# Performance work log

Measured on AMD Instinct MI355X. Metric: run time of the kernel, lower is better.

Reference implementation:

```python
import jax, jax.numpy as jnp
import numpy as np

N_NODES = 50000
N_EDGES = 800000
N_GRAPHS = 64
EPS = 1e-5


def glorot(key, shape):
    fan_in, fan_out = shape[0], shape[1]
    lim = np.sqrt(6.0 / (fan_in + fan_out))
    return jax.random.uniform(key, shape, jnp.float32, -lim, lim)


def setup_inputs() -> dict:
    key = jax.random.key(0)
    ks = jax.random.split(key, 12)
    x = jax.random.normal(ks[0], (N_NODES, 1), jnp.float32)
    edge_index = jax.random.randint(ks[1], (2, N_EDGES), 0, N_NODES, jnp.int64)
    batch = jnp.sort(jax.random.randint(ks[2], (N_NODES,), 0, N_GRAPHS, jnp.int64))
    dims = [(1, 256), (256, 256), (256, 128)]
    params = {}
    for i, (di, do) in enumerate(dims):
        params[f"Wl{i}"] = glorot(ks[3 + 3 * i], (di, do))          # neighbor (lin_l) weight
        params[f"b{i}"] = jnp.zeros((do,), jnp.float32)              # lin_l bias
        params[f"Wr{i}"] = glorot(ks[4 + 3 * i], (di, do))           # root (lin_r) weight
    params["gamma"] = jnp.ones((128,), jnp.float32)
    params["beta"] = jnp.zeros((128,), jnp.float32)
    return {"x": x, "edge_index": edge_index, "batch": batch, **params}


def _sage_conv(x, src, dst, deg_inv, Wl, b, Wr):
    # mean-aggregate messages x[src] at dst, then lin_l(agg) + lin_r(x)
    agg = jax.ops.segment_sum(x[src], dst, num_segments=N_NODES) * deg_inv
    return agg @ Wl + b + x @ Wr


def reference(x, edge_index, batch, Wl0, b0, Wr0, Wl1, b1, Wr1, Wl2, b2, Wr2, gamma, beta):
    src, dst = edge_index[0], edge_index[1]
    deg = jax.ops.segment_sum(jnp.ones((N_EDGES,), x.dtype), dst, num_segments=N_NODES)
    deg_inv = (1.0 / jnp.maximum(deg, 1.0))[:, None]

    h = _sage_conv(x, src, dst, deg_inv, Wl0, b0, Wr0)
    h = jax.nn.relu(h)  # dropout is identity in eval mode
    h = _sage_conv(h, src, dst, deg_inv, Wl1, b1, Wr1)
    h = jax.nn.relu(h)
    h = _sage_conv(h, src, dst, deg_inv, Wl2, b2, Wr2)

    # global mean pool over graphs
    gsum = jax.ops.segment_sum(h, batch, num_segments=N_GRAPHS)
    gcnt = jax.ops.segment_sum(jnp.ones((N_NODES,), h.dtype), batch, num_segments=N_GRAPHS)
    g = gsum / jnp.maximum(gcnt, 1.0)[:, None]

    # LayerNorm over feature dim
    mu = jnp.mean(g, axis=-1, keepdims=True)
    var = jnp.var(g, axis=-1, keepdims=True)
    return (g - mu) * jax.lax.rsqrt(var + EPS) * gamma + beta
```

## Files before the change

kernel.cpp:

```cpp
#include <hip/hip_runtime.h>
#include <stdint.h>

#define NN 50000
#define NE 800000
#define NG 64
#define F1 256
#define NNP 50176
#define NBK 196
#define NBS 392
#define EPB 2048
#define SCB 391
#define PCHUNKS 112
#define PKC 448
#define PSTEPS 7
#define ZR2 128

typedef __bf16 bf16x8 __attribute__((ext_vector_type(8)));
typedef float f32x4 __attribute__((ext_vector_type(4)));

__device__ __forceinline__ float bf2f(unsigned int u) {
  union { float f; unsigned int i; } v; v.i = (u & 0xffffu) << 16; return v.f;
}
__device__ __forceinline__ unsigned short f2bf(float f) {
  union { float f; unsigned int i; } v; v.f = f;
  unsigned int r = v.i + 0x7fffu + ((v.i >> 16) & 1u);
  return (unsigned short)(r >> 16);
}
__device__ __forceinline__ float asf(unsigned int u) {
  union { unsigned int u; float f; } v; v.u = u; return v.f;
}
__device__ __forceinline__ unsigned int asu(float f) {
  union { float f; unsigned int u; } v; v.f = f; return v.u;
}
__device__ __forceinline__ void gload16(const void* g, void* l) {
  __builtin_amdgcn_global_load_lds(
      (const __attribute__((address_space(1))) unsigned int*)g,
      (__attribute__((address_space(3))) unsigned int*)l, 16, 0, 0);
}

__global__ void k_bhist(const int* __restrict__ ei, int* __restrict__ btot_d,
                        int* __restrict__ btot_s) {
  __shared__ int lhd[NBK];
  __shared__ int lhs[NBS];
  for (int i = threadIdx.x; i < NBK; i += 256) lhd[i] = 0;
  for (int i = threadIdx.x; i < NBS; i += 256) lhs[i] = 0;
  __syncthreads();
  for (int e = blockIdx.x * blockDim.x + threadIdx.x; e < NE; e += gridDim.x * blockDim.x) {
    atomicAdd(&lhs[ei[e] >> 7], 1);
    atomicAdd(&lhd[ei[NE + e] >> 8], 1);
  }
  __syncthreads();
  for (int i = threadIdx.x; i < NBK; i += 256) atomicAdd(&btot_d[i], lhd[i]);
  for (int i = threadIdx.x; i < NBS; i += 256) atomicAdd(&btot_s[i], lhs[i]);
}

__global__ void k_bscan(const int* __restrict__ btot_d, const int* __restrict__ btot_s,
                        int* __restrict__ bbase, int* __restrict__ bcur,
                        int* __restrict__ sbase, int* __restrict__ scur,
                        int* __restrict__ rowp) {
  __shared__ int buf[512];
  int t = threadIdx.x;
  int v = (t < NBK) ? btot_d[t] : 0;
  buf[t] = v;
  __syncthreads();
  for (int off = 1; off < 512; off <<= 1) {
    int o = (t >= off) ? buf[t - off] : 0;
    __syncthreads();
    buf[t] += o;
    __syncthreads();
  }
  if (t < NBK) { bbase[t] = buf[t] - v; bcur[t] = buf[t] - v; }
  if (t == NBK - 1) bbase[NBK] = buf[t];
  __syncthreads();
  int v2 = (t < NBS) ? btot_s[t] : 0;
  buf[t] = v2;
  __syncthreads();
  for (int off = 1; off < 512; off <<= 1) {
    int o = (t >= off) ? buf[t - off] : 0;
    __syncthreads();
    buf[t] += o;
    __syncthreads();
  }
  if (t < NBS) { sbase[t] = buf[t] - v2; scur[t] = buf[t] - v2; }
  if (t == NBS - 1) sbase[NBS] = buf[t];
  if (t == 0) rowp[NN] = NE;
}

__global__ __launch_bounds__(256) void k_bscatter(
    const int* __restrict__ ei, const float* __restrict__ x,
    int* __restrict__ bcur, int* __restrict__ scur,
    uint2* __restrict__ recs, unsigned int* __restrict__ srecs) {
  __shared__ int lhd[NBK]; __shared__ int gbd[NBK];
  __shared__ int lhs[NBS]; __shared__ int gbs[NBS];
  int b = blockIdx.x, tid = threadIdx.x;
  int e0 = b * EPB;
  for (int i = tid; i < NBK; i += 256) lhd[i] = 0;
  for (int i = tid; i < NBS; i += 256) lhs[i] = 0;
  __syncthreads();
  unsigned int meta[8]; float xv[8]; int lofd[8]; int bkd[8]; int lofs[8]; int bks[8];
#pragma unroll
  for (int i = 0; i < 8; ++i) {
    int e = e0 + i * 256 + tid;
    bkd[i] = -1;
    if (e < NE) {
      int s = ei[e], d = ei[NE + e];
      bkd[i] = d >> 8; bks[i] = s >> 7;
      meta[i] = (unsigned int)s | ((unsigned int)d << 16);
      xv[i] = x[s];
      lofd[i] = atomicAdd(&lhd[bkd[i]], 1);
      lofs[i] = atomicAdd(&lhs[bks[i]], 1);
    }
  }
  __syncthreads();
  for (int i = tid; i < NBK; i += 256) gbd[i] = atomicAdd(&bcur[i], lhd[i]);
  for (int i = tid; i < NBS; i += 256) gbs[i] = atomicAdd(&scur[i], lhs[i]);
  __syncthreads();
#pragma unroll
  for (int i = 0; i < 8; ++i) {
    if (bkd[i] >= 0) {
      recs[gbd[bkd[i]] + lofd[i]] = make_uint2(meta[i], asu(xv[i]));
      unsigned int s = meta[i] & 0xFFFFu, d = meta[i] >> 16;
      srecs[gbs[bks[i]] + lofs[i]] = d | ((s & 127u) << 16);
    }
  }
}

__global__ __launch_bounds__(256) void k_csr(
    const uint2* __restrict__ recs, const int* __restrict__ bbase,
    const float* __restrict__ x, const int* __restrict__ batch,
    int* __restrict__ rowp, float2* __restrict__ ax,
    int* __restrict__ colx, uint2* __restrict__ dg) {
  __shared__ int cnt[256];
  __shared__ int sc[256];
  __shared__ float xs[256];
  int b = blockIdx.x, tid = threadIdx.x;
  int eb = bbase[b], ee = bbase[b + 1];
  cnt[tid] = 0;
  xs[tid] = 0.0f;
  __syncthreads();
  for (int e = eb + tid; e < ee; e += 256) {
    uint2 r = recs[e];
    int dl = (r.x >> 16) & 255;
    atomicAdd(&cnt[dl], 1);
    atomicAdd(&xs[dl], asf(r.y));
  }
  __syncthreads();
  sc[tid] = cnt[tid];
  __syncthreads();
  for (int off = 1; off < 256; off <<= 1) {
    int o = (tid >= off) ? sc[tid - off] : 0;
    __syncthreads();
    sc[tid] += o;
    __syncthreads();
  }
  int excl = sc[tid] - cnt[tid];
  int i = b * 256 + tid;
  float dinv = 1.0f / fmaxf((float)cnt[tid], 1.0f);
  if (i < NN) {
    rowp[i] = eb + excl;
    ax[i] = make_float2(xs[tid] * dinv, x[i]);
    dg[i] = make_uint2(asu(dinv), (unsigned int)batch[i]);
  }
  __syncthreads();
  sc[tid] = excl;
  __syncthreads();
  for (int e = eb + tid; e < ee; e += 256) {
    uint2 r = recs[e];
    int dl = (r.x >> 16) & 255;
    int s = r.x & 0xFFFF;
    int slot = atomicAdd(&sc[dl], 1);
    colx[eb + slot] = s;
  }
}

__global__ __launch_bounds__(256) void k_csc(
    const unsigned int* __restrict__ srecs, const int* __restrict__ sbase,
    const uint2* __restrict__ dg, const int* __restrict__ batch,
    unsigned int* __restrict__ wgT3u) {
  __shared__ float wgrow[128 * 65];
  __shared__ int sbt[128];
  int b = blockIdx.x, tid = threadIdx.x;
  for (int i = tid; i < 128 * 65; i += 256) wgrow[i] = 0.0f;
  if (tid < 128) {
    int s = b * 128 + tid;
    sbt[tid] = (s < NN) ? batch[s] : -1;
  }
  __syncthreads();
  int eb = sbase[b], ee = sbase[b + 1];
  for (int e = eb + tid; e < ee; e += 256) {
    unsigned int r = srecs[e];
    int d = r & 0xFFFF;
    int sl = (r >> 16) & 127;
    uint2 t = dg[d];
    atomicAdd(&wgrow[sl * 65 + t.y], asf(t.x));
  }
  __syncthreads();
  int s0u = b * 64;
  int k = tid & 63;
  for (int rr = 0; rr < 16; ++rr) {
    int g = rr * 4 + (tid >> 6);
    float w0 = wgrow[(2 * k) * 65 + g];
    float w1 = wgrow[(2 * k + 1) * 65 + g];
    unsigned short h0 = f2bf(w0), h1v = f2bf(w1);
    unsigned short l0 = f2bf(w0 - bf2f(h0)), l1 = f2bf(w1 - bf2f(h1v));
    wgT3u[(size_t)g * (NNP / 2) + s0u + k] = (unsigned int)h0 | ((unsigned int)h1v << 16);
    wgT3u[(size_t)(64 + g) * (NNP / 2) + s0u + k] = (unsigned int)l0 | ((unsigned int)l1 << 16);
  }
  int bv0 = sbt[2 * k], bv1 = sbt[2 * k + 1];
  for (int rr = 0; rr < 16; ++rr) {
    int g = rr * 4 + (tid >> 6);
    unsigned int u = ((bv0 == g) ? 0x3F80u : 0u) | ((bv1 == g) ? 0x3F800000u : 0u);
    wgT3u[(size_t)(128 + g) * (NNP / 2) + s0u + k] = u;
  }
}

__global__ void k_cnt(const int* __restrict__ batch, int* __restrict__ cnt) {
  int g = threadIdx.x;
  if (g >= NG) return;
  int lo = 0, hi = NN;
  while (lo < hi) { int m = (lo + hi) >> 1; if (batch[m] < g) lo = m + 1; else hi = m; }
  int a = lo;
  lo = 0; hi = NN;
  while (lo < hi) { int m = (lo + hi) >> 1; if (batch[m] < g + 1) lo = m + 1; else hi = m; }
  cnt[g] = lo - a;
}

__global__ void k_axe(const int* __restrict__ colx, const float2* __restrict__ ax,
                      float2* __restrict__ axe) {
  int e = blockIdx.x * blockDim.x + threadIdx.x;
  if (e >= NE) return;
  axe[e] = ax[colx[e]];
}

__global__ void k_wprep(const float* __restrict__ Wl1, const float* __restrict__ Wr1,
                        unsigned short* __restrict__ wcat) {
  int t = blockIdx.x * blockDim.x + threadIdx.x;
  if (t >= 256 * 512) return;
  int n = t >> 9, k = t & 511;
  float v = (k < 256) ? Wl1[k * 256 + n] : Wr1[(k - 256) * 256 + n];
  wcat[t] = f2bf(v);
}

__global__ __launch_bounds__(256) void k_agg2(
    const float2* __restrict__ axe, const int* __restrict__ rowp,
    const float* __restrict__ Wl0, const float* __restrict__ b0,
    const float* __restrict__ Wr0, unsigned short* __restrict__ aggb) {
  int wid = threadIdx.x >> 6, lane = threadIdx.x & 63;
  int gw = blockIdx.x * 4 + wid;
  int tw = gridDim.x * 4;
  float wl[4], wr[4], bb[4];
#pragma unroll
  for (int k = 0; k < 4; ++k) {
    wl[k] = Wl0[lane * 4 + k];
    wr[k] = Wr0[lane * 4 + k];
    bb[k] = b0[lane * 4 + k];
  }
  for (int d = gw; d < NN; d += tw) {
    int beg = rowp[d], end = rowp[d + 1];
    float a[4] = {0.f, 0.f, 0.f, 0.f};
    float c[4] = {0.f, 0.f, 0.f, 0.f};
    int e = beg;
    for (; e + 3 < end; e += 4) {
      float2 v0 = axe[e], v1 = axe[e + 1], v2 = axe[e + 2], v3 = axe[e + 3];
#pragma unroll
      for (int k = 0; k < 4; ++k) {
        a[k] += fmaxf(fmaf(v0.x, wl[k], fmaf(v0.y, wr[k], bb[k])), 0.0f);
        c[k] += fmaxf(fmaf(v1.x, wl[k], fmaf(v1.y, wr[k], bb[k])), 0.0f);
        a[k] += fmaxf(fmaf(v2.x, wl[k], fmaf(v2.y, wr[k], bb[k])), 0.0f);
        c[k] += fmaxf(fmaf(v3.x, wl[k], fmaf(v3.y, wr[k], bb[k])), 0.0f);
      }
    }
    for (; e < end; ++e) {
      float2 v0 = axe[e];
#pragma unroll
      for (int k = 0; k < 4; ++k)
        a[k] += fmaxf(fmaf(v0.x, wl[k], fmaf(v0.y, wr[k], bb[k])), 0.0f);
    }
    float dinv = 1.0f / fmaxf((float)(end - beg), 1.0f);
    uint2 o;
    o.x = (unsigned int)f2bf((a[0] + c[0]) * dinv) | ((unsigned int)f2bf((a[1] + c[1]) * dinv) << 16);
    o.y = (unsigned int)f2bf((a[2] + c[2]) * dinv) | ((unsigned int)f2bf((a[3] + c[3]) * dinv) << 16);
    *(uint2*)(aggb + (size_t)d * F1 + lane * 4) = o;
  }
}

#define BM 128
#define BN 128
#define BK 32

__global__ __launch_bounds__(256) void k_gemm1(
    const unsigned short* __restrict__ aggb, const float2* __restrict__ ax,
    const unsigned short* __restrict__ wcat,
    const float* __restrict__ Wl0, const float* __restrict__ b0,
    const float* __restrict__ Wr0, const float* __restrict__ b1,
    unsigned short* __restrict__ h1T) {
  __shared__ unsigned short As[2][BM][BK];
  __shared__ unsigned short Bs[2][BN][BK];
  __shared__ float wl0s[256], wr0s[256], b0s[256];
  int bm = blockIdx.x, ct = blockIdx.y;
  int tid = threadIdx.x;
  int wid = tid >> 6, lane = tid & 63;
  int wr = wid >> 1, wc = wid & 1;
  int rc = lane & 15, kh = lane >> 4;
  int r0 = bm * BM;
  int srow = tid >> 1;
  int sslot = tid & 1;

  wl0s[tid] = Wl0[tid];
  wr0s[tid] = Wr0[tid];
  b0s[tid] = b0[tid];

  int rA = r0 + srow;
  bool rAok = rA < NN;
  float2 axv = rAok ? ax[rA] : make_float2(0.f, 0.f);

  f32x4 acc[4][4] = {};
  int4 ra0, ra1, rb0, rb1;

#define LOAD_A(kt)                                                             \
  do {                                                                         \
    ra0 = make_int4(0, 0, 0, 0); ra1 = make_int4(0, 0, 0, 0);                  \
    if (rAok) {                                                                \
      const int4* s_ = (const int4*)(aggb + (size_t)rA * F1 + (kt) * BK + sslot * 16); \
      ra0 = s_[0]; ra1 = s_[1];                                                \
    }                                                                          \
  } while (0)

#define LOAD_B(kt)                                                             \
  do {                                                                         \
    const int4* t_ = (const int4*)(wcat + (size_t)(ct * BN + srow) * 512 + (kt) * BK + sslot * 16); \
    rb0 = t_[0]; rb1 = t_[1];                                                  \
  } while (0)

#define COMP_A(kt)                                                             \
  do {                                                                         \
    int j0_ = ((kt) - 8) * BK + sslot * 16;                                    \
    unsigned int w_[8];                                                        \
    _Pragma("unroll") for (int q = 0; q < 8; ++q) {                            \
      int j_ = j0_ + 2 * q;                                                    \
      float f0_ = fmaxf(fmaf(axv.x, wl0s[j_], fmaf(axv.y, wr0s[j_], b0s[j_])), 0.0f); \
      float f1_ = fmaxf(fmaf(axv.x, wl0s[j_ + 1], fmaf(axv.y, wr0s[j_ + 1], b0s[j_ + 1])), 0.0f); \
      w_[q] = (unsigned int)f2bf(f0_) | ((unsigned int)f2bf(f1_) << 16);       \
    }                                                                          \
    ra0 = make_int4(w_[0], w_[1], w_[2], w_[3]);                               \
    ra1 = make_int4(w_[4], w_[5], w_[6], w_[7]);                               \
  } while (0)

#define WRITE_AB(buf)                                                          \
  do {                                                                         \
    int sw_ = (srow >> 1) & 3;                                                 \
    int ws0_ = (2 * sslot) ^ sw_;                                              \
    int ws1_ = (2 * sslot + 1) ^ sw_;                                          \
    *(int4*)&As[buf][srow][ws0_ * 8] = ra0;                                    \
    *(int4*)&As[buf][srow][ws1_ * 8] = ra1;                                    \
    *(int4*)&Bs[buf][srow][ws0_ * 8] = rb0;                                    \
    *(int4*)&Bs[buf][srow][ws1_ * 8] = rb1;                                    \
  } while (0)

  LOAD_B(0);
  LOAD_A(0);
  WRITE_AB(0);
  __syncthreads();
  int cur = 0;
  for (int kt = 0; kt < 16; ++kt) {
    if (kt < 15) {
      LOAD_B(kt + 1);
      if (kt + 1 < 8) LOAD_A(kt + 1);
    }
    bf16x8 af[4], bfr[4];
#pragma unroll
    for (int mf = 0; mf < 4; ++mf) {
      int row = wr * 64 + mf * 16 + rc;
      int sl = kh ^ ((row >> 1) & 3);
      af[mf] = *(const bf16x8*)&As[cur][row][sl * 8];
    }
#pragma unroll
    for (int nf = 0; nf < 4; ++nf) {
      int row = wc * 64 + nf * 16 + rc;
      int sl = kh ^ ((row >> 1) & 3);
      bfr[nf] = *(const bf16x8*)&Bs[cur][row][sl * 8];
    }
#pragma unroll
    for (int mf = 0; mf < 4; ++mf)
#pragma unroll
      for (int nf = 0; nf < 4; ++nf)
        acc[mf][nf] = __builtin_amdgcn_mfma_f32_16x16x32_bf16(af[mf], bfr[nf], acc[mf][nf], 0, 0, 0);
    if (kt < 15) {
      if (kt + 1 >= 8) COMP_A(kt + 1);
      WRITE_AB(cur ^ 1);
    }
    __syncthreads();
    cur ^= 1;
  }
#undef LOAD_A
#undef LOAD_B
#undef COMP_A
#undef WRITE_AB

#pragma unroll
  for (int nf = 0; nf < 4; ++nf) {
    int f = ct * BN + wc * 64 + nf * 16 + rc;
    float bias = b1[f];
    size_t frow = (size_t)f * NNP;
#pragma unroll
    for (int mf = 0; mf < 4; ++mf) {
      int s0 = r0 + wr * 64 + mf * 16 + kh * 4;
      f32x4 a = acc[mf][nf];
      unsigned int lo = (unsigned int)f2bf(fmaxf(a[0] + bias, 0.0f)) |
                        ((unsigned int)f2bf(fmaxf(a[1] + bias, 0.0f)) << 16);
      unsigned int hi = (unsigned int)f2bf(fmaxf(a[2] + bias, 0.0f)) |
                        ((unsigned int)f2bf(fmaxf(a[3] + bias, 0.0f)) << 16);
      *(uint2*)(h1T + frow + s0) = make_uint2(lo, hi);
    }
  }
}

__global__ __launch_bounds__(256, 2) void k_poolmm(
    const unsigned short* __restrict__ h1T, const unsigned short* __restrict__ wgT3,
    float* __restrict__ zpart) {
  __shared__ unsigned short SM[2][2048 * 8];
  int bid = blockIdx.x;
  int lbid = (bid & 7) * 56 + (bid >> 3);
  int c = lbid >> 2, fs = lbid & 3;
  int tid = threadIdx.x;
  int w = tid >> 6, lane = tid & 63, rc = lane & 15, kh = lane >> 4;
  int kbase = c * PKC;
  int fbase = fs * 64;

  const unsigned short* gsrc[8];
#pragma unroll
  for (int r = 0; r < 8; ++r) {
    int sIdx = r * 256 + tid;
    if (sIdx < 1536) {
      int row = sIdx >> 3, sl = sIdx & 7;
      gsrc[r] = wgT3 + (size_t)row * NNP + kbase + (sl ^ (row & 7)) * 8;
    } else {
      int row = (sIdx - 1536) >> 3, sl = sIdx & 7;
      gsrc[r] = h1T + (size_t)(fbase + row) * NNP + kbase + (sl ^ (row & 7)) * 8;
    }
  }

  f32x4 acc[12] = {};

#define PSTAGE(buf, t)                                                         \
  do {                                                                         \
    _Pragma("unroll") for (int r = 0; r < 8; ++r)                              \
      gload16(gsrc[r] + (t) * 64, &SM[buf][(r * 256 + w * 64) * 8]);           \
  } while (0)

#define PCOMP(buf)                                                             \
  do {                                                                         \
    _Pragma("unroll") for (int ks = 0; ks < 2; ++ks) {                         \
      int brow = w * 16 + rc;                                                  \
      int bsl = (ks * 4 + kh) ^ (brow & 7);                                    \
      bf16x8 bf = *(const bf16x8*)&SM[buf][(1536 + brow * 8 + bsl) * 8];       \
      _Pragma("unroll") for (int mt = 0; mt < 12; ++mt) {                      \
        int arow = mt * 16 + rc;                                               \
        int asl = (ks * 4 + kh) ^ (arow & 7);                                  \
        bf16x8 af = *(const bf16x8*)&SM[buf][(arow * 8 + asl) * 8];            \
        acc[mt] = __builtin_amdgcn_mfma_f32_16x16x32_bf16(af, bf, acc[mt], 0, 0, 0); \
      }                                                                        \
    }                                                                          \
  } while (0)

  PSTAGE(0, 0);
  __syncthreads();
#pragma unroll
  for (int t = 0; t < PSTEPS; ++t) {
    int buf = t & 1;
    if (t + 1 < PSTEPS) PSTAGE(buf ^ 1, t + 1);
    PCOMP(buf);
    __syncthreads();
  }
#undef PSTAGE
#undef PCOMP

  float* zp = zpart + ((size_t)c * ZR2) * F1 + fbase + w * 16 + rc;
#pragma unroll
  for (int mt = 0; mt < 4; ++mt)
#pragma unroll
    for (int r = 0; r < 4; ++r)
      zp[(size_t)(mt * 16 + kh * 4 + r) * F1] = acc[mt][r] + acc[mt + 4][r];
#pragma unroll
  for (int mt = 8; mt < 12; ++mt)
#pragma unroll
    for (int r = 0; r < 4; ++r)
      zp[(size_t)((mt - 8) * 16 + 64 + kh * 4 + r) * F1] = acc[mt][r];
}

__global__ void k_zred(const float* __restrict__ zpart, float* __restrict__ z,
                       float* __restrict__ p1) {
  int g = blockIdx.x, q = blockIdx.y, t = threadIdx.x;
  float a = 0.0f, b = 0.0f;
  for (int c = q * 14; c < q * 14 + 14; ++c) {
    const float* base = zpart + (size_t)c * ZR2 * F1;
    a += base[(size_t)g * F1 + t];
    b += base[(size_t)(64 + g) * F1 + t];
  }
  atomicAdd(&z[g * F1 + t], a);
  atomicAdd(&p1[g * F1 + t], b);
}

__global__ void k_final(const float* __restrict__ z, const float* __restrict__ p1,
                        const int* __restrict__ cnt,
                        const float* __restrict__ Wl2, const float* __restrict__ b2,
                        const float* __restrict__ Wr2, const float* __restrict__ gamma,
                        const float* __restrict__ beta, float* __restrict__ out) {
  __shared__ float s1[128], s2[128];
  int g = blockIdx.x, j = threadIdx.x;
  float invc = 1.0f / fmaxf((float)cnt[g], 1.0f);
  float acc = 0.0f;
  for (int k = 0; k < 256; ++k) {
    acc += z[g * 256 + k] * Wl2[k * 128 + j] + p1[g * 256 + k] * Wr2[k * 128 + j];
  }
  acc = acc * invc + b2[j];
  s1[j] = acc; s2[j] = acc * acc;
  __syncthreads();
  for (int off = 64; off > 0; off >>= 1) {
    if (j < off) { s1[j] += s1[j + off]; s2[j] += s2[j + off]; }
    __syncthreads();
  }
  float mu = s1[0] / 128.0f;
  float var = s2[0] / 128.0f - mu * mu;
  out[g * 128 + j] = (acc - mu) * rsqrtf(var + 1e-5f) * gamma[j] + beta[j];
}

extern "C" void kernel_launch(void* const* d_in, const int* in_sizes, int n_in,
                              void* d_out, int out_size, void* d_ws, size_t ws_size,
                              hipStream_t stream) {
  const float* x = (const float*)d_in[0];
  const int* ei = (const int*)d_in[1];
  const int* batch = (const int*)d_in[2];
  const float* Wl0 = (const float*)d_in[3];
  const float* b0 = (const float*)d_in[4];
  const float* Wr0 = (const float*)d_in[5];
  const float* Wl1 = (const float*)d_in[6];
  const float* b1 = (const float*)d_in[7];
  const float* Wr1 = (const float*)d_in[8];
  const float* Wl2 = (const float*)d_in[9];
  const float* b2 = (const float*)d_in[10];
  const float* Wr2 = (const float*)d_in[11];
  const float* gamma = (const float*)d_in[12];
  const float* beta = (const float*)d_in[13];
  float* out = (float*)d_out;

  char* p = (char*)d_ws;
  auto alloc = [&](size_t bytes) {
    char* r = p;
    p += (bytes + 511) & ~(size_t)511;
    return r;
  };
  unsigned short* h1T = (unsigned short*)alloc((size_t)F1 * NNP * 2);
  unsigned short* aggb = (unsigned short*)alloc((size_t)NN * F1 * 2);
  float2* axe = (float2*)alloc((size_t)NE * 8);
  int* rowp = (int*)alloc((size_t)(NN + 1) * 4);
  float2* ax = (float2*)alloc((size_t)NN * 8);
  uint2* dg = (uint2*)alloc((size_t)NN * 8);
  int* cnt = (int*)alloc((size_t)NG * 4);
  float* z = (float*)alloc((size_t)NG * F1 * 4);
  float* p1 = (float*)alloc((size_t)NG * F1 * 4);
  unsigned short* wcat = (unsigned short*)alloc((size_t)256 * 512 * 2);
  int* btot_d = (int*)alloc((size_t)NBK * 4);
  int* btot_s = (int*)alloc((size_t)NBS * 4);
  int* bbase = (int*)alloc((size_t)(NBK + 1) * 4);
  int* bcur = (int*)alloc((size_t)NBK * 4);
  int* sbase = (int*)alloc((size_t)(NBS + 1) * 4);
  int* scur = (int*)alloc((size_t)NBS * 4);
  unsigned short* wgT3 = (unsigned short*)alloc((size_t)192 * NNP * 2);
  float* zpart = (float*)alloc((size_t)PCHUNKS * ZR2 * F1 * 4);
  uint2* recs = (uint2*)aggb;
  unsigned int* srecs = (unsigned int*)(aggb + (size_t)NE * 4);
  int* colx = (int*)(aggb + (size_t)NE * 6);

  hipMemsetAsync(btot_d, 0, (size_t)NBK * 4, stream);
  hipMemsetAsync(btot_s, 0, (size_t)NBS * 4, stream);
  hipMemsetAsync(p1, 0, (size_t)NG * F1 * 4, stream);
  hipMemsetAsync(z, 0, (size_t)NG * F1 * 4, stream);

  k_bhist<<<256, 256, 0, stream>>>(ei, btot_d, btot_s);
  k_bscan<<<1, 512, 0, stream>>>(btot_d, btot_s, bbase, bcur, sbase, scur, rowp);
  k_bscatter<<<SCB, 256, 0, stream>>>(ei, x, bcur, scur, recs, srecs);
  k_csr<<<NBK, 256, 0, stream>>>(recs, bbase, x, batch, rowp, ax, colx, dg);
  k_csc<<<NBS, 256, 0, stream>>>(srecs, sbase, dg, batch, (unsigned int*)wgT3);
  k_cnt<<<1, 64, 0, stream>>>(batch, cnt);
  k_axe<<<(NE + 255) / 256, 256, 0, stream>>>(colx, ax, axe);
  k_wprep<<<(256 * 512 + 255) / 256, 256, 0, stream>>>(Wl1, Wr1, wcat);
  k_agg2<<<2048, 256, 0, stream>>>(axe, rowp, Wl0, b0, Wr0, aggb);
  dim3 gg(392, 2);
  k_gemm1<<<gg, 256, 0, stream>>>(aggb, ax, wcat, Wl0, b0, Wr0, b1, h1T);
  k_poolmm<<<4 * PCHUNKS, 256, 0, stream>>>(h1T, wgT3, zpart);
  dim3 zg(NG, 8);
  k_zred<<<zg, 256, 0, stream>>>(zpart, z, p1);
  k_final<<<NG, 128, 0, stream>>>(z, p1, cnt, Wl2, b2, Wr2, gamma, beta, out);
}
```

Measured before the change: 189.2 us.

## Drop edge-gather pre-pass and use direct global-to-LDS loads in GEMM

Removes the k_axe kernel that materialized per-edge ax values, and has k_agg2 gather ax[colx[e]] directly, saving an 800K-element write and re-read. In k_gemm1 the register-staged A/B tile loads become direct global-to-LDS 16-byte loads (gload16) with precomputed swizzled addresses. The ReLU-computed second half of A is now written straight into LDS before the MFMAs instead of after them. aggb is padded to NNP rows and the pad is zeroed so the unguarded DMA stays in bounds. colx gets its own buffer instead of aliasing aggb.

```diff
diff --git a/kernel.cpp b/kernel.cpp
--- a/kernel.cpp
+++ b/kernel.cpp
@@ -225,13 +225,6 @@
   cnt[g] = lo - a;
 }
 
-__global__ void k_axe(const int* __restrict__ colx, const float2* __restrict__ ax,
-                      float2* __restrict__ axe) {
-  int e = blockIdx.x * blockDim.x + threadIdx.x;
-  if (e >= NE) return;
-  axe[e] = ax[colx[e]];
-}
-
 __global__ void k_wprep(const float* __restrict__ Wl1, const float* __restrict__ Wr1,
                         unsigned short* __restrict__ wcat) {
   int t = blockIdx.x * blockDim.x + threadIdx.x;
@@ -242,7 +235,8 @@
 }
 
 __global__ __launch_bounds__(256) void k_agg2(
-    const float2* __restrict__ axe, const int* __restrict__ rowp,
+    const int* __restrict__ colx, const float2* __restrict__ ax,
+    const int* __restrict__ rowp,
     const float* __restrict__ Wl0, const float* __restrict__ b0,
     const float* __restrict__ Wr0, unsigned short* __restrict__ aggb) {
   int wid = threadIdx.x >> 6, lane = threadIdx.x & 63;
@@ -261,7 +255,8 @@
     float c[4] = {0.f, 0.f, 0.f, 0.f};
     int e = beg;
     for (; e + 3 < end; e += 4) {
-      float2 v0 = axe[e], v1 = axe[e + 1], v2 = axe[e + 2], v3 = axe[e + 3];
+      int s0 = colx[e], s1 = colx[e + 1], s2 = colx[e + 2], s3 = colx[e + 3];
+      float2 v0 = ax[s0], v1 = ax[s1], v2 = ax[s2], v3 = ax[s3];
 #pragma unroll
       for (int k = 0; k < 4; ++k) {
         a[k] += fmaxf(fmaf(v0.x, wl[k], fmaf(v0.y, wr[k], bb[k])), 0.0f);
@@ -271,7 +266,7 @@
       }
     }
     for (; e < end; ++e) {
-      float2 v0 = axe[e];
+      float2 v0 = ax[colx[e]];
 #pragma unroll
       for (int k = 0; k < 4; ++k)
         a[k] += fmaxf(fmaf(v0.x, wl[k], fmaf(v0.y, wr[k], bb[k])), 0.0f);
@@ -314,25 +309,34 @@
   bool rAok = rA < NN;
   float2 axv = rAok ? ax[rA] : make_float2(0.f, 0.f);
 
+  const unsigned short* gsa[2];
+  const unsigned short* gsb[2];
+  int ldst[2];
+#pragma unroll
+  for (int j = 0; j < 2; ++j) {
+    int sIdx = wid * 128 + j * 64 + lane;
+    int row = sIdx >> 2, phys = sIdx & 3;
+    int sl = phys ^ ((row >> 1) & 3);
+    gsa[j] = aggb + (size_t)(r0 + row) * F1 + sl * 8;
+    gsb[j] = wcat + (size_t)(ct * BN + row) * 512 + sl * 8;
+    ldst[j] = (wid * 128 + j * 64) * 8;
+  }
+
   f32x4 acc[4][4] = {};
-  int4 ra0, ra1, rb0, rb1;
-
-#define LOAD_A(kt)                                                             \
+
+#define DMA_A(buf, kt)                                                         \
   do {                                                                         \
-    ra0 = make_int4(0, 0, 0, 0); ra1 = make_int4(0, 0, 0, 0);                  \
-    if (rAok) {                                                                \
-      const int4* s_ = (const int4*)(aggb + (size_t)rA * F1 + (kt) * BK + sslot * 16); \
-      ra0 = s_[0]; ra1 = s_[1];                                                \
-    }                                                                          \
+    gload16(gsa[0] + (kt) * 32, &As[buf][0][0] + ldst[0]);                     \
+    gload16(gsa[1] + (kt) * 32, &As[buf][0][0] + ldst[1]);                     \
   } while (0)
 
-#define LOAD_B(kt)                                                             \
+#define DMA_B(buf, kt)                                                         \
   do {                                                                         \
-    const int4* t_ = (const int4*)(wcat + (size_t)(ct * BN + srow) * 512 + (kt) * BK + sslot * 16); \
-    rb0 = t_[0]; rb1 = t_[1];                                                  \
+    gload16(gsb[0] + (kt) * 32, &Bs[buf][0][0] + ldst[0]);                     \
+    gload16(gsb[1] + (kt) * 32, &Bs[buf][0][0] + ldst[1]);                     \
   } while (0)
 
-#define COMP_A(kt)                                                             \
+#define COMPW_A(buf, kt)                                                       \
   do {                                                                         \
     int j0_ = ((kt) - 8) * BK + sslot * 16;                                    \
     unsigned int w_[8];                                                        \
@@ -342,30 +346,20 @@
       float f1_ = fmaxf(fmaf(axv.x, wl0s[j_ + 1], fmaf(axv.y, wr0s[j_ + 1], b0s[j_ + 1])), 0.0f); \
       w_[q] = (unsigned int)f2bf(f0_) | ((unsigned int)f2bf(f1_) << 16);       \
     }                                                                          \
-    ra0 = make_int4(w_[0], w_[1], w_[2], w_[3]);                               \
-    ra1 = make_int4(w_[4], w_[5], w_[6], w_[7]);                               \
+    int sw_ = (srow >> 1) & 3;                                                 \
+    *(int4*)&As[buf][srow][((2 * sslot) ^ sw_) * 8] = make_int4(w_[0], w_[1], w_[2], w_[3]); \
+    *(int4*)&As[buf][srow][((2 * sslot + 1) ^ sw_) * 8] = make_int4(w_[4], w_[5], w_[6], w_[7]); \
   } while (0)
 
-#define WRITE_AB(buf)                                                          \
-  do {                                                                         \
-    int sw_ = (srow >> 1) & 3;                                                 \
-    int ws0_ = (2 * sslot) ^ sw_;                                              \
-    int ws1_ = (2 * sslot + 1) ^ sw_;                                          \
-    *(int4*)&As[buf][srow][ws0_ * 8] = ra0;                                    \
-    *(int4*)&As[buf][srow][ws1_ * 8] = ra1;                                    \
-    *(int4*)&Bs[buf][srow][ws0_ * 8] = rb0;                                    \
-    *(int4*)&Bs[buf][srow][ws1_ * 8] = rb1;                                    \
-  } while (0)
-
-  LOAD_B(0);
-  LOAD_A(0);
-  WRITE_AB(0);
+  DMA_A(0, 0);
+  DMA_B(0, 0);
   __syncthreads();
   int cur = 0;
   for (int kt = 0; kt < 16; ++kt) {
     if (kt < 15) {
-      LOAD_B(kt + 1);
-      if (kt + 1 < 8) LOAD_A(kt + 1);
+      DMA_B(cur ^ 1, kt + 1);
+      if (kt + 1 < 8) DMA_A(cur ^ 1, kt + 1);
+      else COMPW_A(cur ^ 1, kt + 1);
     }
     bf16x8 af[4], bfr[4];
 #pragma unroll
@@ -385,17 +379,12 @@
 #pragma unroll
       for (int nf = 0; nf < 4; ++nf)
         acc[mf][nf] = __builtin_amdgcn_mfma_f32_16x16x32_bf16(af[mf], bfr[nf], acc[mf][nf], 0, 0, 0);
-    if (kt < 15) {
-      if (kt + 1 >= 8) COMP_A(kt + 1);
-      WRITE_AB(cur ^ 1);
-    }
     __syncthreads();
     cur ^= 1;
   }
-#undef LOAD_A
-#undef LOAD_B
-#undef COMP_A
-#undef WRITE_AB
+#undef DMA_A
+#undef DMA_B
+#undef COMPW_A
 
 #pragma unroll
   for (int nf = 0; nf < 4; ++nf) {
@@ -551,8 +540,8 @@
     return r;
   };
   unsigned short* h1T = (unsigned short*)alloc((size_t)F1 * NNP * 2);
-  unsigned short* aggb = (unsigned short*)alloc((size_t)NN * F1 * 2);
-  float2* axe = (float2*)alloc((size_t)NE * 8);
+  unsigned short* aggb = (unsigned short*)alloc((size_t)NNP * F1 * 2);
+  int* colx = (int*)alloc((size_t)NE * 4);
   int* rowp = (int*)alloc((size_t)(NN + 1) * 4);
   float2* ax = (float2*)alloc((size_t)NN * 8);
   uint2* dg = (uint2*)alloc((size_t)NN * 8);
@@ -570,12 +559,12 @@
   float* zpart = (float*)alloc((size_t)PCHUNKS * ZR2 * F1 * 4);
   uint2* recs = (uint2*)aggb;
   unsigned int* srecs = (unsigned int*)(aggb + (size_t)NE * 4);
-  int* colx = (int*)(aggb + (size_t)NE * 6);
 
   hipMemsetAsync(btot_d, 0, (size_t)NBK * 4, stream);
   hipMemsetAsync(btot_s, 0, (size_t)NBS * 4, stream);
   hipMemsetAsync(p1, 0, (size_t)NG * F1 * 4, stream);
   hipMemsetAsync(z, 0, (size_t)NG * F1 * 4, stream);
+  hipMemsetAsync(aggb + (size_t)NN * F1, 0, (size_t)(NNP - NN) * F1 * 2, stream);
 
   k_bhist<<<256, 256, 0, stream>>>(ei, btot_d, btot_s);
   k_bscan<<<1, 512, 0, stream>>>(btot_d, btot_s, bbase, bcur, sbase, scur, rowp);
@@ -583,9 +572,8 @@
   k_csr<<<NBK, 256, 0, stream>>>(recs, bbase, x, batch, rowp, ax, colx, dg);
   k_csc<<<NBS, 256, 0, stream>>>(srecs, sbase, dg, batch, (unsigned int*)wgT3);
   k_cnt<<<1, 64, 0, stream>>>(batch, cnt);
-  k_axe<<<(NE + 255) / 256, 256, 0, stream>>>(colx, ax, axe);
   k_wprep<<<(256 * 512 + 255) / 256, 256, 0, stream>>>(Wl1, Wr1, wcat);
-  k_agg2<<<2048, 256, 0, stream>>>(axe, rowp, Wl0, b0, Wr0, aggb);
+  k_agg2<<<2048, 256, 0, stream>>>(colx, ax, rowp, Wl0, b0, Wr0, aggb);
   dim3 gg(392, 2);
   k_gemm1<<<gg, 256, 0, stream>>>(aggb, ax, wcat, Wl0, b0, Wr0, b1, h1T);
   k_poolmm<<<4 * PCHUNKS, 256, 0, stream>>>(h1T, wgT3, zpart);
```

New measurement: 194.0 us. 1.03x slower.
